# Optimization experiments

Measured on AMD Instinct MI355X. Metric: run time of the kernel, lower is better.

## Reference

```python
import jax, jax.numpy as jnp
import numpy as np

B = 32        # decode batch size (live requests)
H = 32        # query heads
HKV = 8       # kv heads (GQA group = H // HKV = 4)
D = 128       # head dim
P = 16        # page size (tokens per page)
M = 128       # max pages per (slot, kv_head) -> max context M*P = 2048
SLOTS = 32    # cache slots
NUM_PAGES = SLOTS * HKV * M
LMAX = M * P
SCALE = 0.08838834764831845  # 1/sqrt(D)


def setup_inputs() -> dict:
    key = jax.random.key(0)
    k0, k1, k2, k3, k4, k5 = jax.random.split(key, 6)
    return {
        "q": jax.random.normal(k0, (B, H, D), dtype=jnp.float32),
        "k": jax.random.normal(k1, (B, HKV, D), dtype=jnp.float32),
        "v": jax.random.normal(k2, (B, HKV, D), dtype=jnp.float32),
        "k_cache": jax.random.normal(k3, (NUM_PAGES, P, D), dtype=jnp.float32),
        "v_cache": jax.random.normal(k4, (NUM_PAGES, P, D), dtype=jnp.float32),
        "bh_seq_lens": jax.random.randint(k5, (SLOTS, HKV), 0, 1500, dtype=jnp.int32),
        "page_table": jnp.arange(SLOTS * HKV * M, dtype=jnp.int32).reshape(SLOTS, HKV, M),
        "batch_mapping": jnp.arange(B, dtype=jnp.int32),
    }


def reference(q, k, v, k_cache, v_cache, bh_seq_lens, page_table, batch_mapping):
    # --- gather per-batch state (self.bh_seq_lens.index_select(0, batch_mapping)) ---
    seq_lens = bh_seq_lens[batch_mapping]          # [B, HKV] per-(req, kv_head) lens
    pt = page_table[batch_mapping]                 # [B, HKV, M] page ids

    # --- decode_store_kv: scatter the new token's k/v into the paged cache ---
    page_of_pos = jnp.take_along_axis(pt, (seq_lens // P)[..., None], axis=-1)[..., 0]  # [B, HKV]
    flat_slot = page_of_pos.astype(jnp.int32) * P + (seq_lens % P)                      # [B, HKV]
    kc = k_cache.reshape(-1, D).at[flat_slot.reshape(-1)].set(k.reshape(-1, D))
    vc = v_cache.reshape(-1, D).at[flat_slot.reshape(-1)].set(v.reshape(-1, D))
    new_lens = seq_lens + 1                        # [B, HKV]

    # --- head_sparse_decode_attention: gather paged KV per (req, kv_head) ---
    tok_idx = (pt[..., None].astype(jnp.int32) * P + jnp.arange(P, dtype=jnp.int32))
    tok_idx = tok_idx.reshape(B, HKV, LMAX)        # flat token slots per (b, h)
    keys = kc[tok_idx]                             # [B, HKV, LMAX, D]
    vals = vc[tok_idx]                             # [B, HKV, LMAX, D]

    # GQA: group query heads onto kv heads
    qg = q.reshape(B, HKV, H // HKV, D)            # [B, HKV, G, D]
    scores = jnp.einsum('bhgd,bhld->bhgl', qg, keys) * SCALE
    valid = jnp.arange(LMAX, dtype=jnp.int32)[None, None, :] < new_lens[..., None]  # [B, HKV, LMAX]
    scores = jnp.where(valid[:, :, None, :], scores, -jnp.inf)
    probs = jax.nn.softmax(scores, axis=-1)
    o = jnp.einsum('bhgl,bhld->bhgd', probs, vals).reshape(B, H, D)
    return o
```

## Files before the change

kernel.cpp:

```cpp
#include <hip/hip_runtime.h>

#define NB 32
#define NH 32
#define NHKV 8
#define NG 4
#define ND 128
#define NP 16
#define NM 128
#define CH 128
#define MAXC 12

template<int CTRL>
__device__ __forceinline__ float dppf(float x) {
    return __builtin_bit_cast(float,
        __builtin_amdgcn_update_dpp(0, __builtin_bit_cast(int, x), CTRL, 0xF, 0xF, true));
}
#define DPP_XOR1  0xB1
#define DPP_XOR2  0x4E
#define DPP_BC0   0x00
#define DPP_BC1   0x55
#define DPP_BC2   0xAA
#define DPP_BC3   0xFF
#define DPP_ROR4  0x124
#define DPP_ROR8  0x128


__global__ __launch_bounds__(256, 4)
void pa_chunk(const float* __restrict__ q,
              const float* __restrict__ knew,
              const float* __restrict__ vnew,
              const float* __restrict__ kc,
              const float* __restrict__ vc,
              const int* __restrict__ bh_seq_lens,
              const int* __restrict__ page_table,
              const int* __restrict__ batch_mapping,
              float* __restrict__ ws_o,
              float* __restrict__ ws_l,
              float* __restrict__ out)
{
    __shared__ int s_pages[CH / NP];
    __shared__ __align__(16) float s_part[4][NG][ND];
    __shared__ float s_sums[4][NG];

    const int bh = blockIdx.x;
    const int c  = blockIdx.y;
    const int b = bh >> 3;
    const int h = bh & 7;
    const int slot = batch_mapping[b];
    const int seq = bh_seq_lens[slot * NHKV + h];
    const int L = seq + 1;
    const int t0 = c * CH;
    if (t0 >= L) return;
    const int n = min(CH, L - t0);
    const int nc = (L + CH - 1) / CH;
    const int* pt = page_table + (slot * NHKV + h) * NM;

    const int tid = threadIdx.x;
    const int l16 = tid & 15;
    const int grp = tid >> 4;

    if (tid < CH / NP) s_pages[tid] = pt[(t0 >> 4) + tid];

    float4 qa[NG], qb[NG];
    #pragma unroll
    for (int g = 0; g < NG; ++g) {
        const float* qp = q + (size_t)(b * NH + h * NG + g) * ND;
        qa[g] = *reinterpret_cast<const float4*>(qp + 4 * l16);
        qb[g] = *reinterpret_cast<const float4*>(qp + 64 + 4 * l16);
    }

    const float4* kc4 = reinterpret_cast<const float4*>(kc);
    const float4* vc4 = reinterpret_cast<const float4*>(vc);
    const float4* knew4 = reinterpret_cast<const float4*>(knew);
    const float4* vnew4 = reinterpret_cast<const float4*>(vnew);
    const float scale = 0.08838834764831845f;

    __syncthreads();

    float4 oa[NG] = {{0,0,0,0},{0,0,0,0},{0,0,0,0},{0,0,0,0}};
    float4 ob[NG] = {{0,0,0,0},{0,0,0,0},{0,0,0,0},{0,0,0,0}};
    float psum = 0.f;

    auto proc = [&](const float4 ka, const float4 kb,
                    const float4 va, const float4 vb, const bool act) {
        float a0 = qa[0].x*ka.x + qa[0].y*ka.y + qa[0].z*ka.z + qa[0].w*ka.w
                 + qb[0].x*kb.x + qb[0].y*kb.y + qb[0].z*kb.z + qb[0].w*kb.w;
        float a1 = qa[1].x*ka.x + qa[1].y*ka.y + qa[1].z*ka.z + qa[1].w*ka.w
                 + qb[1].x*kb.x + qb[1].y*kb.y + qb[1].z*kb.z + qb[1].w*kb.w;
        float a2 = qa[2].x*ka.x + qa[2].y*ka.y + qa[2].z*ka.z + qa[2].w*ka.w
                 + qb[2].x*kb.x + qb[2].y*kb.y + qb[2].z*kb.z + qb[2].w*kb.w;
        float a3 = qa[3].x*ka.x + qa[3].y*ka.y + qa[3].z*ka.z + qa[3].w*ka.w
                 + qb[3].x*kb.x + qb[3].y*kb.y + qb[3].z*kb.z + qb[3].w*kb.w;
        a0 += dppf<DPP_XOR1>(a0); a1 += dppf<DPP_XOR1>(a1);
        a2 += dppf<DPP_XOR1>(a2); a3 += dppf<DPP_XOR1>(a3);
        a0 += dppf<DPP_XOR2>(a0); a1 += dppf<DPP_XOR2>(a1);
        a2 += dppf<DPP_XOR2>(a2); a3 += dppf<DPP_XOR2>(a3);
        float s = (l16 & 2) ? ((l16 & 1) ? a3 : a2) : ((l16 & 1) ? a1 : a0);
        s += dppf<DPP_ROR4>(s);
        s += dppf<DPP_ROR8>(s);
        const float pe = act ? __expf(s * scale) : 0.f;
        psum += pe;
        const float p0 = dppf<DPP_BC0>(pe);
        const float p1 = dppf<DPP_BC1>(pe);
        const float p2 = dppf<DPP_BC2>(pe);
        const float p3 = dppf<DPP_BC3>(pe);
        oa[0].x += p0*va.x; oa[0].y += p0*va.y; oa[0].z += p0*va.z; oa[0].w += p0*va.w;
        ob[0].x += p0*vb.x; ob[0].y += p0*vb.y; ob[0].z += p0*vb.z; ob[0].w += p0*vb.w;
        oa[1].x += p1*va.x; oa[1].y += p1*va.y; oa[1].z += p1*va.z; oa[1].w += p1*va.w;
        ob[1].x += p1*vb.x; ob[1].y += p1*vb.y; ob[1].z += p1*vb.z; ob[1].w += p1*vb.w;
        oa[2].x += p2*va.x; oa[2].y += p2*va.y; oa[2].z += p2*va.z; oa[2].w += p2*va.w;
        ob[2].x += p2*vb.x; ob[2].y += p2*vb.y; ob[2].z += p2*vb.z; ob[2].w += p2*vb.w;
        oa[3].x += p3*va.x; oa[3].y += p3*va.y; oa[3].z += p3*va.z; oa[3].w += p3*va.w;
        ob[3].x += p3*vb.x; ob[3].y += p3*vb.y; ob[3].z += p3*vb.z; ob[3].w += p3*vb.w;
    };

    const bool last_chunk = (t0 + CH >= L);

    if (!last_chunk) {
        size_t r = ((size_t)s_pages[0] * NP + grp) * 32 + l16;
        float4 ka = kc4[r], kb = kc4[r + 16];
        float4 va = vc4[r], vb = vc4[r + 16];
        #pragma unroll 2
        for (int p = 0; p < CH / NP - 1; ++p) {
            const size_t rn = ((size_t)s_pages[p + 1] * NP + grp) * 32 + l16;
            const float4 nka = kc4[rn], nkb = kc4[rn + 16];
            const float4 nva = vc4[rn], nvb = vc4[rn + 16];
            proc(ka, kb, va, vb, true);
            ka = nka; kb = nkb; va = nva; vb = nvb;
        }
        proc(ka, kb, va, vb, true);
    } else {
        const int nf = (n - 1) & ~(NP - 1);
        for (int p = 0; p < (nf >> 4); ++p) {
            const size_t row = ((size_t)s_pages[p] * NP + grp) * 32 + l16;
            const float4 ka = kc4[row];
            const float4 kb = kc4[row + 16];
            const float4 va = vc4[row];
            const float4 vb = vc4[row + 16];
            proc(ka, kb, va, vb, true);
        }
        {
            const int t = nf + grp;
            const int gt = t0 + t;
            const bool act = (t < n);
            const bool isnew = (gt == seq);
            const float4* kptr = isnew ? knew4 : kc4;
            const float4* vptr = isnew ? vnew4 : vc4;
            const size_t row = isnew ? (size_t)(b * NHKV + h) * 32
                                     : ((size_t)s_pages[t >> 4] * NP + (t & 15)) * 32;
            const float4 ka = kptr[row + l16];
            const float4 kb = kptr[row + 16 + l16];
            const float4 va = vptr[row + l16];
            const float4 vb = vptr[row + 16 + l16];
            proc(ka, kb, va, vb, act);
        }
    }

    #pragma unroll
    for (int g = 0; g < NG; ++g) {
        oa[g].x += __shfl_xor(oa[g].x, 16); oa[g].y += __shfl_xor(oa[g].y, 16);
        oa[g].z += __shfl_xor(oa[g].z, 16); oa[g].w += __shfl_xor(oa[g].w, 16);
        ob[g].x += __shfl_xor(ob[g].x, 16); ob[g].y += __shfl_xor(ob[g].y, 16);
        ob[g].z += __shfl_xor(ob[g].z, 16); ob[g].w += __shfl_xor(ob[g].w, 16);
        oa[g].x += __shfl_xor(oa[g].x, 32); oa[g].y += __shfl_xor(oa[g].y, 32);
        oa[g].z += __shfl_xor(oa[g].z, 32); oa[g].w += __shfl_xor(oa[g].w, 32);
        ob[g].x += __shfl_xor(ob[g].x, 32); ob[g].y += __shfl_xor(ob[g].y, 32);
        ob[g].z += __shfl_xor(ob[g].z, 32); ob[g].w += __shfl_xor(ob[g].w, 32);
    }
    psum += __shfl_xor(psum, 16);
    psum += __shfl_xor(psum, 32);

    const int wv = tid >> 6;
    if ((tid & 63) < 16) {
        #pragma unroll
        for (int g = 0; g < NG; ++g) {
            *reinterpret_cast<float4*>(&s_part[wv][g][4 * l16]) = oa[g];
            *reinterpret_cast<float4*>(&s_part[wv][g][64 + 4 * l16]) = ob[g];
        }
    }
    if ((tid & 63) < NG) s_sums[wv][tid & 3] = psum;
    __syncthreads();

    if (nc == 1) {
        for (int idx = tid; idx < NG * ND; idx += 256) {
            const int g = idx >> 7;
            const int d = idx & 127;
            const float num = s_part[0][g][d] + s_part[1][g][d] + s_part[2][g][d] + s_part[3][g][d];
            const float den = s_sums[0][g] + s_sums[1][g] + s_sums[2][g] + s_sums[3][g];
            out[(size_t)(b * NH + h * NG + g) * ND + d] = num / den;
        }
        return;
    }

    for (int idx = tid; idx < NG * ND; idx += 256) {
        const int g = idx >> 7;
        const int d = idx & 127;
        ws_o[((size_t)(bh * MAXC + c) * NG + g) * ND + d] =
            s_part[0][g][d] + s_part[1][g][d] + s_part[2][g][d] + s_part[3][g][d];
    }
    if (tid < NG) {
        ws_l[(size_t)(bh * MAXC + c) * NG + tid] =
            s_sums[0][tid] + s_sums[1][tid] + s_sums[2][tid] + s_sums[3][tid];
    }
}

__global__ __launch_bounds__(512, 2)
void pa_combine(const float* __restrict__ ws_o,
                const float* __restrict__ ws_l,
                const int* __restrict__ bh_seq_lens,
                const int* __restrict__ batch_mapping,
                float* __restrict__ out)
{
    const int bh = blockIdx.x;
    const int b = bh >> 3;
    const int h = bh & 7;
    const int L = bh_seq_lens[batch_mapping[b] * NHKV + h] + 1;
    const int nc = (L + CH - 1) / CH;
    if (nc == 1) return;

    const int tid = threadIdx.x;
    const int g = tid >> 7;
    const int d = tid & 127;

    float num = 0.f, den = 0.f;
    #pragma unroll
    for (int c = 0; c < MAXC; ++c) {
        if (c < nc) {
            num += ws_o[((size_t)(bh * MAXC + c) * NG + g) * ND + d];
            den += ws_l[(size_t)(bh * MAXC + c) * NG + g];
        }
    }
    out[(size_t)(b * NH + h * NG + g) * ND + d] = num / den;
}

extern "C" void kernel_launch(void* const* d_in, const int* in_sizes, int n_in,
                              void* d_out, int out_size, void* d_ws, size_t ws_size,
                              hipStream_t stream) {
    const float* q    = (const float*)d_in[0];
    const float* knew = (const float*)d_in[1];
    const float* vnew = (const float*)d_in[2];
    const float* kc   = (const float*)d_in[3];
    const float* vc   = (const float*)d_in[4];
    const int* seqls  = (const int*)d_in[5];
    const int* ptab   = (const int*)d_in[6];
    const int* bmap   = (const int*)d_in[7];
    float* out        = (float*)d_out;

    float* ws_o = (float*)d_ws;
    float* ws_l = ws_o + (size_t)NB * NHKV * MAXC * NG * ND;

    dim3 grid(NB * NHKV, MAXC);
    pa_chunk<<<grid, 256, 0, stream>>>(q, knew, vnew, kc, vc, seqls, ptab, bmap,
                                       ws_o, ws_l, out);
    pa_combine<<<NB * NHKV, 512, 0, stream>>>(ws_o, ws_l, seqls, bmap, out);
}
```

Before: 45.08 us.

## Deepen KV prefetch pipeline, prescale q, and hoist tail-token loads

Full chunks now keep three pages of K/V loads in flight through a four-slot register ring, instead of the single-page double buffer used before. Partial chunks issue the tail-token loads before the page loop and software-pipeline the page loop. q is multiplied by the softmax scale once at load time, which removes a multiply per score. The extra live registers need a lower launch-bounds occupancy target (3 instead of 4 blocks), trading occupancy for memory-level parallelism within each thread.

```diff
diff --git a/kernel.cpp b/kernel.cpp
--- a/kernel.cpp
+++ b/kernel.cpp
@@ -25,7 +25,7 @@
 #define DPP_ROR8  0x128
 
 
-__global__ __launch_bounds__(256, 4)
+__global__ __launch_bounds__(256, 3)
 void pa_chunk(const float* __restrict__ q,
               const float* __restrict__ knew,
               const float* __restrict__ vnew,
@@ -61,19 +61,23 @@
 
     if (tid < CH / NP) s_pages[tid] = pt[(t0 >> 4) + tid];
 
+    const float scale = 0.08838834764831845f;
+
     float4 qa[NG], qb[NG];
     #pragma unroll
     for (int g = 0; g < NG; ++g) {
         const float* qp = q + (size_t)(b * NH + h * NG + g) * ND;
-        qa[g] = *reinterpret_cast<const float4*>(qp + 4 * l16);
-        qb[g] = *reinterpret_cast<const float4*>(qp + 64 + 4 * l16);
+        float4 ta = *reinterpret_cast<const float4*>(qp + 4 * l16);
+        float4 tb = *reinterpret_cast<const float4*>(qp + 64 + 4 * l16);
+        ta.x *= scale; ta.y *= scale; ta.z *= scale; ta.w *= scale;
+        tb.x *= scale; tb.y *= scale; tb.z *= scale; tb.w *= scale;
+        qa[g] = ta; qb[g] = tb;
     }
 
     const float4* kc4 = reinterpret_cast<const float4*>(kc);
     const float4* vc4 = reinterpret_cast<const float4*>(vc);
     const float4* knew4 = reinterpret_cast<const float4*>(knew);
     const float4* vnew4 = reinterpret_cast<const float4*>(vnew);
-    const float scale = 0.08838834764831845f;
 
     __syncthreads();
 
@@ -98,7 +102,7 @@
         float s = (l16 & 2) ? ((l16 & 1) ? a3 : a2) : ((l16 & 1) ? a1 : a0);
         s += dppf<DPP_ROR4>(s);
         s += dppf<DPP_ROR8>(s);
-        const float pe = act ? __expf(s * scale) : 0.f;
+        const float pe = act ? __expf(s) : 0.f;
         psum += pe;
         const float p0 = dppf<DPP_BC0>(pe);
         const float p1 = dppf<DPP_BC1>(pe);
@@ -117,43 +121,52 @@
     const bool last_chunk = (t0 + CH >= L);
 
     if (!last_chunk) {
-        size_t r = ((size_t)s_pages[0] * NP + grp) * 32 + l16;
-        float4 ka = kc4[r], kb = kc4[r + 16];
-        float4 va = vc4[r], vb = vc4[r + 16];
-        #pragma unroll 2
-        for (int p = 0; p < CH / NP - 1; ++p) {
-            const size_t rn = ((size_t)s_pages[p + 1] * NP + grp) * 32 + l16;
-            const float4 nka = kc4[rn], nkb = kc4[rn + 16];
-            const float4 nva = vc4[rn], nvb = vc4[rn + 16];
-            proc(ka, kb, va, vb, true);
-            ka = nka; kb = nkb; va = nva; vb = nvb;
-        }
-        proc(ka, kb, va, vb, true);
+        float4 Ka[4], Kb[4], Va[4], Vb[4];
+        #pragma unroll
+        for (int p = 0; p < 3; ++p) {
+            const size_t r = ((size_t)s_pages[p] * NP + grp) * 32 + l16;
+            Ka[p] = kc4[r]; Kb[p] = kc4[r + 16];
+            Va[p] = vc4[r]; Vb[p] = vc4[r + 16];
+        }
+        #pragma unroll
+        for (int p = 0; p < CH / NP; ++p) {
+            if (p + 3 < CH / NP) {
+                const size_t r = ((size_t)s_pages[p + 3] * NP + grp) * 32 + l16;
+                Ka[(p + 3) & 3] = kc4[r]; Kb[(p + 3) & 3] = kc4[r + 16];
+                Va[(p + 3) & 3] = vc4[r]; Vb[(p + 3) & 3] = vc4[r + 16];
+            }
+            proc(Ka[p & 3], Kb[p & 3], Va[p & 3], Vb[p & 3], true);
+        }
     } else {
         const int nf = (n - 1) & ~(NP - 1);
-        for (int p = 0; p < (nf >> 4); ++p) {
-            const size_t row = ((size_t)s_pages[p] * NP + grp) * 32 + l16;
-            const float4 ka = kc4[row];
-            const float4 kb = kc4[row + 16];
-            const float4 va = vc4[row];
-            const float4 vb = vc4[row + 16];
+
+        const int t = nf + grp;
+        const bool act = (t < n);
+        const bool isnew = (t0 + t == seq);
+        const float4* kp = isnew ? knew4 : kc4;
+        const float4* vp = isnew ? vnew4 : vc4;
+        const size_t trow = isnew ? (size_t)(b * NHKV + h) * 32
+                                  : ((size_t)s_pages[t >> 4] * NP + (t & 15)) * 32;
+        const float4 tka = kp[trow + l16];
+        const float4 tkb = kp[trow + 16 + l16];
+        const float4 tva = vp[trow + l16];
+        const float4 tvb = vp[trow + 16 + l16];
+
+        const int npg = nf >> 4;
+        if (npg > 0) {
+            size_t r = ((size_t)s_pages[0] * NP + grp) * 32 + l16;
+            float4 ka = kc4[r], kb = kc4[r + 16];
+            float4 va = vc4[r], vb = vc4[r + 16];
+            for (int p = 0; p + 1 < npg; ++p) {
+                const size_t rn = ((size_t)s_pages[p + 1] * NP + grp) * 32 + l16;
+                const float4 nka = kc4[rn], nkb = kc4[rn + 16];
+                const float4 nva = vc4[rn], nvb = vc4[rn + 16];
+                proc(ka, kb, va, vb, true);
+                ka = nka; kb = nkb; va = nva; vb = nvb;
+            }
             proc(ka, kb, va, vb, true);
         }
-        {
-            const int t = nf + grp;
-            const int gt = t0 + t;
-            const bool act = (t < n);
-            const bool isnew = (gt == seq);
-            const float4* kptr = isnew ? knew4 : kc4;
-            const float4* vptr = isnew ? vnew4 : vc4;
-            const size_t row = isnew ? (size_t)(b * NHKV + h) * 32
-                                     : ((size_t)s_pages[t >> 4] * NP + (t & 15)) * 32;
-            const float4 ka = kptr[row + l16];
-            const float4 kb = kptr[row + 16 + l16];
-            const float4 va = vptr[row + l16];
-            const float4 vb = vptr[row + 16 + l16];
-            proc(ka, kb, va, vb, act);
-        }
+        proc(tka, tkb, tva, tvb, act);
     }
 
     #pragma unroll
```

Measured after the change: 50.07 us. +11.1%, slower.
